# Performance work log

Measured on AMD Instinct MI355X. Metric: run time of the kernel, lower is better.

## Reference

```python
import jax, jax.numpy as jnp
import numpy as np

N, E = 50000, 800000          # nodes, edges
IN, OUT, ED = 128, 64, 32     # in_dim, out_dim, edge_dim


def setup_inputs() -> dict:
    key = jax.random.key(0)
    ks = jax.random.split(key, 8)
    init = lambda k, shape, fan: jax.random.normal(k, shape, jnp.float32) * np.float32(1.0 / np.sqrt(fan))
    return {
        "x": jax.random.normal(ks[0], (N, IN), jnp.float32),
        "edge_attr": jax.random.normal(ks[1], (E, ED), jnp.float32),
        "edge_index": jax.random.randint(ks[2], (2, E), 0, N),
        "W_fc": init(ks[3], (IN, OUT), IN),
        "b_fc": jnp.zeros((OUT,), jnp.float32),
        "W_attn": init(ks[4], (2 * OUT + ED, 1), 2 * OUT + ED),
        "b_attn": jnp.zeros((1,), jnp.float32),
        "W_edge": init(ks[5], (ED, OUT), ED),
        "b_edge": jnp.zeros((OUT,), jnp.float32),
        "W_self": init(ks[6], (IN, OUT), IN),
        "b_self": jnp.zeros((OUT,), jnp.float32),
    }


def reference(x, edge_attr, edge_index, W_fc, b_fc, W_attn, b_attn,
              W_edge, b_edge, W_self, b_self):
    row, col = edge_index[0], edge_index[1]   # src, dst node ids per edge
    # node transform: z = fc(x)  (batch norm disabled -> identity)
    z = x @ W_fc + b_fc                        # [N, OUT]
    # edge-dependent attention logits: cat(z_src, z_dst, ex) -> scalar
    z2 = jnp.concatenate([z[row], z[col], edge_attr], axis=1)   # [E, 2*OUT+ED]
    e = jax.nn.leaky_relu(z2 @ W_attn + b_attn, negative_slope=0.2)  # [E, 1]
    # edge feature transform for aggregation
    ez = edge_attr @ W_edge + b_edge           # [E, OUT]
    # segment softmax over incoming edges of each destination node
    m = jax.ops.segment_max(e, col, num_segments=N)   # [N, 1]
    m = jnp.where(jnp.isfinite(m), m, 0.0)             # nodes with no in-edges
    p = jnp.exp(e - m[col])                             # [E, 1]
    denom = jax.ops.segment_sum(p, col, num_segments=N)
    alpha = p / jnp.maximum(denom[col], 1e-16)          # [E, 1]
    # attention-weighted aggregation of node messages + edge messages
    h = jax.ops.segment_sum(alpha * (z[row] + ez), col, num_segments=N)  # [N, OUT]
    # self-loop residual with its own transform
    h = h + (x @ W_self + b_self)
    return h
```

## Files before the change

kernel.cpp:

```cpp
#include <hip/hip_runtime.h>

typedef unsigned int uint;
typedef unsigned short u16;

#define IN_DIM 128
#define OUT_DIM 64
#define ED_DIM 32
#define CAP 64

typedef __bf16 bf16x8 __attribute__((ext_vector_type(8)));
typedef float f32x4 __attribute__((ext_vector_type(4)));

static __device__ __forceinline__ float bf2f(u16 u) {
    return __uint_as_float(((uint)u) << 16);
}
static __device__ __forceinline__ u16 f2bf(float f) {
    uint u = __float_as_uint(f);
    uint r = u + 0x7fffu + ((u >> 16) & 1u);
    return (u16)(r >> 16);
}
static __device__ __forceinline__ float ldf(const void* p, size_t i, bool f32m) {
    return f32m ? ((const float*)p)[i] : bf2f(((const u16*)p)[i]);
}

__global__ __launch_bounds__(256) void k0_prep(
    const u16* __restrict__ xraw, const void* __restrict__ Wfc,
    const void* __restrict__ Wself, u16* __restrict__ Wt_fc,
    u16* __restrict__ Wt_s, uint* __restrict__ flag)
{
    __shared__ int cnt;
    if (threadIdx.x == 0) cnt = 0;
    __syncthreads();
    float v = bf2f(xraw[threadIdx.x]);
    if (!(fabsf(v) <= 64.f)) atomicAdd(&cnt, 1);
    __syncthreads();
    bool f32m = cnt > 0;
    if (threadIdx.x == 0) flag[0] = f32m ? 1u : 0u;
    for (int i = threadIdx.x; i < IN_DIM * OUT_DIM; i += 256) {
        int j = i & 7, lane = (i >> 3) & 63, frag = i >> 9;
        int kt = frag >> 2, nt = frag & 3;
        int q = lane >> 4, c = lane & 15;
        int k = kt * 32 + q * 8 + j;
        int n = nt * 16 + c;
        int src = k * OUT_DIM + n;
        Wt_fc[i] = f32m ? f2bf(((const float*)Wfc)[src]) : ((const u16*)Wfc)[src];
        Wt_s [i] = f32m ? f2bf(((const float*)Wself)[src]) : ((const u16*)Wself)[src];
    }
}

__global__ __launch_bounds__(256) void k1_mfma(
    const void* __restrict__ x, const u16* __restrict__ Wt_fc,
    const u16* __restrict__ Wt_s, const void* __restrict__ bfc,
    const void* __restrict__ Wattn, const void* __restrict__ bself,
    u16* __restrict__ z_bf, float* __restrict__ hself,
    float* __restrict__ a_src, float* __restrict__ a_dst,
    uint* __restrict__ cursor, const uint* __restrict__ flag, int n_nodes)
{
    bool f32m = flag[0] != 0u;
    int tid = blockIdx.x * 256 + threadIdx.x;
    int stride = gridDim.x * 256;
    for (int i = tid; i < n_nodes; i += stride) cursor[i] = 0u;

    int wave = threadIdx.x >> 6, lane = threadIdx.x & 63;
    int q = lane >> 4, c = lane & 15;
    int nb = blockIdx.x * 64 + wave * 16;
    if (nb >= n_nodes) return;

    f32x4 az[4], as_[4];
    #pragma unroll
    for (int nt = 0; nt < 4; nt++) {
        az[nt]  = (f32x4){0.f, 0.f, 0.f, 0.f};
        as_[nt] = (f32x4){0.f, 0.f, 0.f, 0.f};
    }

    int m = nb + c; if (m >= n_nodes) m = n_nodes - 1;

    #pragma unroll
    for (int kt = 0; kt < 4; kt++) {
        int k0 = kt * 32 + q * 8;
        bf16x8 a;
        if (f32m) {
            const float* xr = (const float*)x + (size_t)m * IN_DIM + k0;
            float4 f0 = *(const float4*)xr;
            float4 f1 = *(const float4*)(xr + 4);
            a[0] = (__bf16)f0.x; a[1] = (__bf16)f0.y; a[2] = (__bf16)f0.z; a[3] = (__bf16)f0.w;
            a[4] = (__bf16)f1.x; a[5] = (__bf16)f1.y; a[6] = (__bf16)f1.z; a[7] = (__bf16)f1.w;
        } else {
            a = *(const bf16x8*)((const u16*)x + (size_t)m * IN_DIM + k0);
        }
        #pragma unroll
        for (int nt = 0; nt < 4; nt++) {
            int fo = ((kt * 4 + nt) * 64 + lane) * 8;
            bf16x8 bf = *(const bf16x8*)(Wt_fc + fo);
            bf16x8 bs = *(const bf16x8*)(Wt_s + fo);
            az[nt]  = __builtin_amdgcn_mfma_f32_16x16x32_bf16(a, bf, az[nt], 0, 0, 0);
            as_[nt] = __builtin_amdgcn_mfma_f32_16x16x32_bf16(a, bs, as_[nt], 0, 0, 0);
        }
    }

    float was[4], wad[4], bz[4], bs[4];
    #pragma unroll
    for (int nt = 0; nt < 4; nt++) {
        was[nt] = ldf(Wattn, nt * 16 + c, f32m);
        wad[nt] = ldf(Wattn, 64 + nt * 16 + c, f32m);
        bz[nt]  = ldf(bfc, nt * 16 + c, f32m);
        bs[nt]  = ldf(bself, nt * 16 + c, f32m);
    }
    #pragma unroll
    for (int reg = 0; reg < 4; reg++) {
        int nn = nb + q * 4 + reg;
        bool ok = nn < n_nodes;
        float ps = 0.f, pd = 0.f;
        #pragma unroll
        for (int nt = 0; nt < 4; nt++) {
            float zv = az[nt][reg] + bz[nt];
            float hv = as_[nt][reg] + bs[nt];
            float zp = __shfl_xor(zv, 1, 64);
            if (ok) {
                hself[(size_t)nn * OUT_DIM + nt * 16 + c] = hv;
                if (!(c & 1)) {
                    uint u = (uint)f2bf(zv) | ((uint)f2bf(zp) << 16);
                    *(uint*)(z_bf + (size_t)nn * OUT_DIM + nt * 16 + c) = u;
                }
            }
            ps = fmaf(zv, was[nt], ps);
            pd = fmaf(zv, wad[nt], pd);
        }
        #pragma unroll
        for (int off = 8; off; off >>= 1) {
            ps += __shfl_xor(ps, off, 64);
            pd += __shfl_xor(pd, off, 64);
        }
        if (ok && c == 0) { a_src[nn] = ps; a_dst[nn] = pd; }
    }
}

__global__ __launch_bounds__(256) void k4_scatter(
    const int* __restrict__ ei, const void* __restrict__ edge_attr,
    const void* __restrict__ Wattn, const void* __restrict__ battn,
    const float* __restrict__ a_src, const float* __restrict__ a_dst,
    uint* __restrict__ cursor, uint2* __restrict__ meta,
    u16* __restrict__ ea_bf, const uint* __restrict__ flag,
    int use_ea, int n_edges)
{
    bool f32m = flag[0] != 0u;
    int e = blockIdx.x * 256 + threadIdx.x;
    if (e >= n_edges) return;
    int r = ei[e];
    int c = ei[n_edges + e];
    float s = a_src[r] + a_dst[c] + ldf(battn, 0, f32m);

    uint wpk[16];
    if (f32m) {
        const float* ea = (const float*)edge_attr + (size_t)e * ED_DIM;
        const float* wa = (const float*)Wattn + 128;
        #pragma unroll
        for (int j = 0; j < 16; j++) {
            float v0 = ea[2 * j], v1 = ea[2 * j + 1];
            s = fmaf(v0, wa[2 * j], fmaf(v1, wa[2 * j + 1], s));
            wpk[j] = (uint)f2bf(v0) | ((uint)f2bf(v1) << 16);
        }
    } else {
        const uint* ea = (const uint*)((const u16*)edge_attr + (size_t)e * ED_DIM);
        const u16* wa = (const u16*)Wattn + 128;
        #pragma unroll
        for (int j = 0; j < 16; j++) {
            uint u = ea[j];
            s = fmaf(__uint_as_float(u << 16), bf2f(wa[2 * j]),
                fmaf(__uint_as_float(u & 0xffff0000u), bf2f(wa[2 * j + 1]), s));
            wpk[j] = u;
        }
    }
    float l = s > 0.f ? s : 0.2f * s;
    float p = __expf(l);
    uint pos = atomicAdd(&cursor[c], 1u);
    if (pos < CAP)
        meta[((size_t)c << 6) + pos] = make_uint2((uint)e, __float_as_uint(p));
    if (use_ea) {
        uint4* dst = (uint4*)(ea_bf + (size_t)e * ED_DIM);
        dst[0] = make_uint4(wpk[0], wpk[1], wpk[2], wpk[3]);
        dst[1] = make_uint4(wpk[4], wpk[5], wpk[6], wpk[7]);
        dst[2] = make_uint4(wpk[8], wpk[9], wpk[10], wpk[11]);
        dst[3] = make_uint4(wpk[12], wpk[13], wpk[14], wpk[15]);
    }
}

__global__ __launch_bounds__(256) void k5_agg(
    const int* __restrict__ ei, const void* __restrict__ edge_attr,
    const void* __restrict__ Wedge, const void* __restrict__ bedge,
    const u16* __restrict__ z_bf, const float* __restrict__ hself,
    const uint* __restrict__ cursor, const uint2* __restrict__ meta,
    const u16* __restrict__ ea_bf, void* __restrict__ out,
    const uint* __restrict__ flag, int use_ea, int n_nodes)
{
    bool f32m = flag[0] != 0u;
    __shared__ float sWedge[ED_DIM * OUT_DIM];
    for (int i = threadIdx.x; i < ED_DIM * OUT_DIM; i += 256)
        sWedge[i] = ldf(Wedge, i, f32m);
    __syncthreads();

    int lane = threadIdx.x & 63;
    int n = (blockIdx.x * 256 + threadIdx.x) >> 6;
    if (n >= n_nodes) return;

    uint deg = cursor[n];
    if (deg > CAP) deg = CAP;
    float h = hself[(size_t)n * OUT_DIM + lane];

    if (deg > 0) {
        int l32 = lane & 31;
        bool hi = lane >= 32;
        const uint2* seg = meta + ((size_t)n << 6);
        float d = 0.f, accz = 0.f, accea = 0.f;

        for (uint i = 0; i < deg; i += 4) {
            uint j1 = (i + 1 < deg) ? i + 1 : i;
            uint j2 = (i + 2 < deg) ? i + 2 : i;
            uint j3 = (i + 3 < deg) ? i + 3 : j2;
            bool vA = hi ? (i + 1 < deg) : true;
            bool vB = hi ? (i + 3 < deg) : (i + 2 < deg);
            uint2 mA = seg[hi ? j1 : i];
            uint2 mB = seg[hi ? j3 : j2];
            float pA = vA ? __uint_as_float(mA.y) : 0.f;
            float pB = vB ? __uint_as_float(mB.y) : 0.f;
            uint rA = (uint)ei[mA.x];
            uint rB = (uint)ei[mB.x];
            float eavA = use_ea ? bf2f(ea_bf[(size_t)mA.x * ED_DIM + l32])
                                : ldf(edge_attr, (size_t)mA.x * ED_DIM + l32, f32m);
            float eavB = use_ea ? bf2f(ea_bf[(size_t)mB.x * ED_DIM + l32])
                                : ldf(edge_attr, (size_t)mB.x * ED_DIM + l32, f32m);
            accea = fmaf(pA, eavA, fmaf(pB, eavB, accea));

            float pAo = __shfl_xor(pA, 32, 64);
            float pBo = __shfl_xor(pB, 32, 64);
            uint  rAo = __shfl_xor(rA, 32, 64);
            uint  rBo = __shfl_xor(rB, 32, 64);
            float p0 = hi ? pAo : pA, p1 = hi ? pA : pAo;
            float p2 = hi ? pBo : pB, p3 = hi ? pB : pBo;
            uint  r0 = hi ? rAo : rA, r1 = hi ? rA : rAo;
            uint  r2 = hi ? rBo : rB, r3 = hi ? rB : rBo;
            float z0 = bf2f(z_bf[(size_t)r0 * OUT_DIM + lane]);
            float z1 = bf2f(z_bf[(size_t)r1 * OUT_DIM + lane]);
            float z2 = bf2f(z_bf[(size_t)r2 * OUT_DIM + lane]);
            float z3 = bf2f(z_bf[(size_t)r3 * OUT_DIM + lane]);
            d += (p0 + p1) + (p2 + p3);
            accz = fmaf(p0, z0, fmaf(p1, z1, fmaf(p2, z2, fmaf(p3, z3, accz))));
        }
        accea += __shfl_xor(accea, 32, 64);

        float inv = 1.f / fmaxf(d, 1e-30f);
        float hea = accea * inv;
        float he = ldf(bedge, lane, f32m);
        #pragma unroll 8
        for (int j = 0; j < ED_DIM; j++) {
            float hj = __shfl(hea, j, 64);
            he = fmaf(hj, sWedge[j * OUT_DIM + lane], he);
        }
        h += accz * inv + he;
    }

    size_t oi = (size_t)n * OUT_DIM + lane;
    if (f32m) ((float*)out)[oi] = h;
    else      ((u16*)out)[oi] = f2bf(h);
}

extern "C" void kernel_launch(void* const* d_in, const int* in_sizes, int n_in,
                              void* d_out, int out_size, void* d_ws, size_t ws_size,
                              hipStream_t stream) {
    const void* x         = d_in[0];
    const void* edge_attr = d_in[1];
    const int*  ei        = (const int*)d_in[2];
    const void* Wfc       = d_in[3];
    const void* bfc       = d_in[4];
    const void* Wattn     = d_in[5];
    const void* battn     = d_in[6];
    const void* Wedge     = d_in[7];
    const void* bedge     = d_in[8];
    const void* Wself     = d_in[9];
    const void* bself     = d_in[10];

    const int N = in_sizes[0] / IN_DIM;
    const int E = in_sizes[1] / ED_DIM;

    char* ws = (char*)d_ws;
    size_t off = 0;
    auto alloc = [&](size_t bytes) -> void* {
        void* p = ws + off;
        off += (bytes + 255) & ~(size_t)255;
        return p;
    };
    u16*   z_bf   = (u16*)  alloc((size_t)N * OUT_DIM * sizeof(u16));
    float* hself  = (float*)alloc((size_t)N * OUT_DIM * sizeof(float));
    float* a_src  = (float*)alloc((size_t)N * sizeof(float));
    float* a_dst  = (float*)alloc((size_t)N * sizeof(float));
    uint*  cursor = (uint*) alloc((size_t)N * sizeof(uint));
    uint2* meta   = (uint2*)alloc((size_t)N * CAP * sizeof(uint2));
    u16*   Wt_fc  = (u16*)  alloc((size_t)IN_DIM * OUT_DIM * sizeof(u16));
    u16*   Wt_s   = (u16*)  alloc((size_t)IN_DIM * OUT_DIM * sizeof(u16));
    uint*  flag   = (uint*) alloc(256);

    size_t ea_bytes = (size_t)E * ED_DIM * sizeof(u16);
    int use_ea = (off + ea_bytes + 4096 <= ws_size) ? 1 : 0;
    u16* ea_bf = use_ea ? (u16*)alloc(ea_bytes) : (u16*)ws;

    int mfmaBlocks = (N + 63) / 64;
    int nodeBlocks = (N + 3) / 4;
    int edgeBlocks = (E + 255) / 256;

    k0_prep<<<1, 256, 0, stream>>>((const u16*)x, Wfc, Wself, Wt_fc, Wt_s, flag);
    k1_mfma<<<mfmaBlocks, 256, 0, stream>>>(x, Wt_fc, Wt_s, bfc, Wattn, bself,
                                            z_bf, hself, a_src, a_dst,
                                            cursor, flag, N);
    k4_scatter<<<edgeBlocks, 256, 0, stream>>>(ei, edge_attr, Wattn, battn,
                                               a_src, a_dst, cursor,
                                               meta, ea_bf, flag, use_ea, E);
    k5_agg<<<nodeBlocks, 256, 0, stream>>>(ei, edge_attr, Wedge, bedge,
                                           z_bf, hself, cursor, meta, ea_bf,
                                           d_out, flag, use_ea, N);
}
```

Measured before the change: 346.6 us.

## Preload edge metadata per lane and broadcast via readlane in aggregation

Result: faster. 332.0 us (-4.2%).

```diff
diff --git a/kernel.cpp b/kernel.cpp
--- a/kernel.cpp
+++ b/kernel.cpp
@@ -21,6 +21,12 @@
 }
 static __device__ __forceinline__ float ldf(const void* p, size_t i, bool f32m) {
     return f32m ? ((const float*)p)[i] : bf2f(((const u16*)p)[i]);
+}
+static __device__ __forceinline__ float rlanef(float v, int l) {
+    return __uint_as_float((uint)__builtin_amdgcn_readlane((int)__float_as_uint(v), l));
+}
+static __device__ __forceinline__ uint rlaneu(uint v, int l) {
+    return (uint)__builtin_amdgcn_readlane((int)v, l);
 }
 
 __global__ __launch_bounds__(256) void k0_prep(
@@ -148,18 +154,26 @@
     if (e >= n_edges) return;
     int r = ei[e];
     int c = ei[n_edges + e];
+    uint pos = atomicAdd(&cursor[c], 1u);
     float s = a_src[r] + a_dst[c] + ldf(battn, 0, f32m);
 
-    uint wpk[16];
     if (f32m) {
         const float* ea = (const float*)edge_attr + (size_t)e * ED_DIM;
         const float* wa = (const float*)Wattn + 128;
+        uint wpk[16];
         #pragma unroll
         for (int j = 0; j < 16; j++) {
             float v0 = ea[2 * j], v1 = ea[2 * j + 1];
             s = fmaf(v0, wa[2 * j], fmaf(v1, wa[2 * j + 1], s));
             wpk[j] = (uint)f2bf(v0) | ((uint)f2bf(v1) << 16);
         }
+        if (use_ea) {
+            uint4* dst = (uint4*)(ea_bf + (size_t)e * ED_DIM);
+            dst[0] = make_uint4(wpk[0], wpk[1], wpk[2], wpk[3]);
+            dst[1] = make_uint4(wpk[4], wpk[5], wpk[6], wpk[7]);
+            dst[2] = make_uint4(wpk[8], wpk[9], wpk[10], wpk[11]);
+            dst[3] = make_uint4(wpk[12], wpk[13], wpk[14], wpk[15]);
+        }
     } else {
         const uint* ea = (const uint*)((const u16*)edge_attr + (size_t)e * ED_DIM);
         const u16* wa = (const u16*)Wattn + 128;
@@ -168,21 +182,12 @@
             uint u = ea[j];
             s = fmaf(__uint_as_float(u << 16), bf2f(wa[2 * j]),
                 fmaf(__uint_as_float(u & 0xffff0000u), bf2f(wa[2 * j + 1]), s));
-            wpk[j] = u;
         }
     }
     float l = s > 0.f ? s : 0.2f * s;
     float p = __expf(l);
-    uint pos = atomicAdd(&cursor[c], 1u);
     if (pos < CAP)
         meta[((size_t)c << 6) + pos] = make_uint2((uint)e, __float_as_uint(p));
-    if (use_ea) {
-        uint4* dst = (uint4*)(ea_bf + (size_t)e * ED_DIM);
-        dst[0] = make_uint4(wpk[0], wpk[1], wpk[2], wpk[3]);
-        dst[1] = make_uint4(wpk[4], wpk[5], wpk[6], wpk[7]);
-        dst[2] = make_uint4(wpk[8], wpk[9], wpk[10], wpk[11]);
-        dst[3] = make_uint4(wpk[12], wpk[13], wpk[14], wpk[15]);
-    }
 }
 
 __global__ __launch_bounds__(256) void k5_agg(
@@ -208,52 +213,62 @@
     float h = hself[(size_t)n * OUT_DIM + lane];
 
     if (deg > 0) {
+        const uint2* seg = meta + ((size_t)n << 6);
+        bool act = (uint)lane < deg;
+        float p_l = 0.f;
+        uint eid_l = 0u, row_l = 0u;
+        if (act) {
+            uint2 me = seg[lane];
+            p_l = __uint_as_float(me.y);
+            eid_l = me.x;
+            row_l = (uint)ei[me.x];
+        }
+
+        float d = p_l;
+        #pragma unroll
+        for (int off = 32; off; off >>= 1) d += __shfl_xor(d, off, 64);
+
         int l32 = lane & 31;
-        bool hi = lane >= 32;
-        const uint2* seg = meta + ((size_t)n << 6);
-        float d = 0.f, accz = 0.f, accea = 0.f;
-
-        for (uint i = 0; i < deg; i += 4) {
-            uint j1 = (i + 1 < deg) ? i + 1 : i;
-            uint j2 = (i + 2 < deg) ? i + 2 : i;
-            uint j3 = (i + 3 < deg) ? i + 3 : j2;
-            bool vA = hi ? (i + 1 < deg) : true;
-            bool vB = hi ? (i + 3 < deg) : (i + 2 < deg);
-            uint2 mA = seg[hi ? j1 : i];
-            uint2 mB = seg[hi ? j3 : j2];
-            float pA = vA ? __uint_as_float(mA.y) : 0.f;
-            float pB = vB ? __uint_as_float(mB.y) : 0.f;
-            uint rA = (uint)ei[mA.x];
-            uint rB = (uint)ei[mB.x];
-            float eavA = use_ea ? bf2f(ea_bf[(size_t)mA.x * ED_DIM + l32])
-                                : ldf(edge_attr, (size_t)mA.x * ED_DIM + l32, f32m);
-            float eavB = use_ea ? bf2f(ea_bf[(size_t)mB.x * ED_DIM + l32])
-                                : ldf(edge_attr, (size_t)mB.x * ED_DIM + l32, f32m);
-            accea = fmaf(pA, eavA, fmaf(pB, eavB, accea));
-
-            float pAo = __shfl_xor(pA, 32, 64);
-            float pBo = __shfl_xor(pB, 32, 64);
-            uint  rAo = __shfl_xor(rA, 32, 64);
-            uint  rBo = __shfl_xor(rB, 32, 64);
-            float p0 = hi ? pAo : pA, p1 = hi ? pA : pAo;
-            float p2 = hi ? pBo : pB, p3 = hi ? pB : pBo;
-            uint  r0 = hi ? rAo : rA, r1 = hi ? rA : rAo;
-            uint  r2 = hi ? rBo : rB, r3 = hi ? rB : rBo;
-            float z0 = bf2f(z_bf[(size_t)r0 * OUT_DIM + lane]);
-            float z1 = bf2f(z_bf[(size_t)r1 * OUT_DIM + lane]);
-            float z2 = bf2f(z_bf[(size_t)r2 * OUT_DIM + lane]);
-            float z3 = bf2f(z_bf[(size_t)r3 * OUT_DIM + lane]);
-            d += (p0 + p1) + (p2 + p3);
-            accz = fmaf(p0, z0, fmaf(p1, z1, fmaf(p2, z2, fmaf(p3, z3, accz))));
+        int hi = lane >> 5;
+        const float* eaf = (const float*)edge_attr;
+        const u16* eab = f32m ? ea_bf : (const u16*)edge_attr;
+        bool ea_f32 = f32m && !use_ea;
+
+        float accz = 0.f, accea = 0.f;
+        uint pad8 = (deg + 7u) & ~7u;
+        for (uint j = 0; j < pad8; j += 8) {
+            float pz[8]; uint rz[8], gz[8];
+            #pragma unroll
+            for (int t = 0; t < 8; t++) {
+                pz[t] = rlanef(p_l, (int)(j + t));
+                rz[t] = rlaneu(row_l, (int)(j + t));
+                gz[t] = rlaneu(eid_l, (int)(j + t));
+            }
+            float z[8];
+            #pragma unroll
+            for (int t = 0; t < 8; t++)
+                z[t] = bf2f(z_bf[(size_t)rz[t] * OUT_DIM + lane]);
+            float va[4], pa[4];
+            #pragma unroll
+            for (int t = 0; t < 4; t++) {
+                uint g = hi ? gz[2 * t + 1] : gz[2 * t];
+                pa[t] = hi ? pz[2 * t + 1] : pz[2 * t];
+                va[t] = ea_f32 ? eaf[(size_t)g * ED_DIM + l32]
+                               : bf2f(eab[(size_t)g * ED_DIM + l32]);
+            }
+            #pragma unroll
+            for (int t = 0; t < 8; t++) accz = fmaf(pz[t], z[t], accz);
+            #pragma unroll
+            for (int t = 0; t < 4; t++) accea = fmaf(pa[t], va[t], accea);
         }
         accea += __shfl_xor(accea, 32, 64);
 
         float inv = 1.f / fmaxf(d, 1e-30f);
         float hea = accea * inv;
         float he = ldf(bedge, lane, f32m);
-        #pragma unroll 8
+        #pragma unroll
         for (int j = 0; j < ED_DIM; j++) {
-            float hj = __shfl(hea, j, 64);
+            float hj = rlanef(hea, j);
             he = fmaf(hj, sWedge[j * OUT_DIM + lane], he);
         }
         h += accz * inv + he;
```
